# Performance work log

Measured on AMD Instinct MI355X. Metric: run time of the kernel, lower is better.

The kernel has to match this reference:

```python
import jax, jax.numpy as jnp
import numpy as np

H = 16
D_MODEL = 1024
D_K = D_MODEL // H
NWORDS = 16384


def setup_inputs() -> dict:
    key0 = jax.random.key(0)
    ks = jax.random.split(key0, 11)
    s = 0.02
    return {
        "query": jax.random.normal(ks[0], (1, D_MODEL), dtype=jnp.float32),
        "key": jax.random.normal(ks[1], (NWORDS, D_MODEL), dtype=jnp.float32),
        "value": jax.random.normal(ks[2], (NWORDS, D_MODEL), dtype=jnp.float32),
        "Wq": jax.random.normal(ks[3], (D_MODEL, D_MODEL), dtype=jnp.float32) * s,
        "bq": jax.random.normal(ks[4], (D_MODEL,), dtype=jnp.float32) * s,
        "Wk": jax.random.normal(ks[5], (D_MODEL, D_MODEL), dtype=jnp.float32) * s,
        "bk": jax.random.normal(ks[6], (D_MODEL,), dtype=jnp.float32) * s,
        "Wv": jax.random.normal(ks[7], (D_MODEL, D_MODEL), dtype=jnp.float32) * s,
        "bv": jax.random.normal(ks[8], (D_MODEL,), dtype=jnp.float32) * s,
        "Wo": jax.random.normal(ks[9], (D_MODEL, D_MODEL), dtype=jnp.float32) * s,
        "bo": jax.random.normal(ks[10], (D_MODEL,), dtype=jnp.float32) * s,
    }


def reference(query, key, value, Wq, bq, Wk, bk, Wv, bv, Wo, bo):
    # torch Linear: y = x @ W.T + b
    q = (query @ Wq.T + bq).reshape(H, D_K)          # [h, d_k]  (single query token)
    k = (key @ Wk.T + bk).reshape(-1, H, D_K)        # [n, h, d_k]
    v = (value @ Wv.T + bv).reshape(-1, H, D_K)      # [n, h, d_k]
    # NOTE: original module applies NO 1/sqrt(d_k) scaling.
    scores = jnp.einsum("hd,nhd->hn", q, k)          # [h, n]
    p_attn = jax.nn.softmax(scores, axis=-1)          # dropout p=0 -> no-op
    x = jnp.einsum("hn,nhd->hd", p_attn, v).reshape(1, H * D_K)  # [1, d_model]
    return x @ Wo.T + bo                              # [1, d_model]
```

## Files before the change

kernel.cpp:

```cpp
#include <hip/hip_runtime.h>

#define DM 1024
#define NW 16384

typedef __attribute__((ext_vector_type(8))) short short8;
typedef __attribute__((ext_vector_type(4))) float f32x4;

#define OFF_AH   1024
#define OFF_AL   9216
#define OFF_D0   17408
#define OFF_SP   17440
#define OFF_X    25632
#define OFF_W    26656
#define OFF_PART 49152

__device__ __forceinline__ unsigned short f2bf(float f) {
  unsigned int u = __float_as_uint(f);
  return (unsigned short)((u + 0x7fffu + ((u >> 16) & 1u)) >> 16);
}

__global__ __launch_bounds__(256) void k_rowdot(const float* __restrict__ W,
                                                const float* __restrict__ v,
                                                const float* __restrict__ b,
                                                float* __restrict__ out) {
  const int wave = (blockIdx.x * 256 + threadIdx.x) >> 6;
  const int lane = threadIdx.x & 63;
  const float* row = W + (size_t)wave * DM + 4 * lane;
  float s = 0.f;
#pragma unroll
  for (int j = 0; j < 4; ++j) {
    float4 a = *(const float4*)(row + j * 256);
    float4 x = *(const float4*)(v + j * 256 + 4 * lane);
    s += a.x * x.x + a.y * x.y + a.z * x.z + a.w * x.w;
  }
#pragma unroll
  for (int off = 32; off; off >>= 1) s += __shfl_xor(s, off, 64);
  if (lane == 0) out[wave] = s + b[wave];
}

__global__ __launch_bounds__(256) void k_qck(const float* __restrict__ Wq,
                                             const float* __restrict__ bq,
                                             const float* __restrict__ query,
                                             const float* __restrict__ Wk,
                                             const float* __restrict__ bk,
                                             short* __restrict__ Ah,
                                             short* __restrict__ Al,
                                             float* __restrict__ d0,
                                             float* __restrict__ w) {
  const int h = blockIdx.x >> 2;
  const int mc = blockIdx.x & 3;
  const int t = threadIdx.x;
  const int lane = t & 63;
  const int wv = t >> 6;
  __shared__ float qh[64];
  w[blockIdx.x * 256 + t] = 0.f;
  float4 qv[4];
#pragma unroll
  for (int j = 0; j < 4; ++j) qv[j] = *(const float4*)(query + j * 256 + 4 * lane);
#pragma unroll 1
  for (int ii = 0; ii < 16; ii += 4) {
    float4 a[4][4];
#pragma unroll
    for (int r = 0; r < 4; ++r) {
      const float* rp = Wq + (size_t)(h * 64 + 4 * (ii + r) + wv) * DM + 4 * lane;
#pragma unroll
      for (int j = 0; j < 4; ++j) a[r][j] = *(const float4*)(rp + j * 256);
    }
    float s[4] = {0.f, 0.f, 0.f, 0.f};
#pragma unroll
    for (int r = 0; r < 4; ++r)
#pragma unroll
      for (int j = 0; j < 4; ++j)
        s[r] += a[r][j].x * qv[j].x + a[r][j].y * qv[j].y +
                a[r][j].z * qv[j].z + a[r][j].w * qv[j].w;
#pragma unroll
    for (int off = 32; off; off >>= 1)
#pragma unroll
      for (int r = 0; r < 4; ++r) s[r] += __shfl_xor(s[r], off, 64);
    if (lane == 0)
#pragma unroll
      for (int r = 0; r < 4; ++r)
        qh[4 * (ii + r) + wv] = s[r] + bq[h * 64 + 4 * (ii + r) + wv];
  }
  __syncthreads();
  const int m = mc * 256 + t;
  const float* Wp = Wk + (size_t)(h * 64) * DM + m;
  float s = 0.f;
#pragma unroll 2
  for (int db = 0; db < 8; ++db) {
    float wv8[8];
#pragma unroll
    for (int j = 0; j < 8; ++j) wv8[j] = Wp[(size_t)(db * 8 + j) * DM];
#pragma unroll
    for (int j = 0; j < 8; ++j) s = fmaf(qh[db * 8 + j], wv8[j], s);
  }
  unsigned short hu = f2bf(s);
  float hf = __uint_as_float(((unsigned int)hu) << 16);
  unsigned short lu = f2bf(s - hf);
  const int kb = m >> 5, q = (m >> 3) & 3, j = m & 7;
  const int idx = (kb * 64 + q * 16 + h) * 8 + j;
  Ah[idx] = (short)hu;
  Al[idx] = (short)lu;
  if (mc == 0 && t == 0) {
    float tt = 0.f;
    for (int d = 0; d < 64; ++d) tt += qh[d] * bk[h * 64 + d];
    d0[h] = tt;
  }
}

__global__ __launch_bounds__(512, 4) void k_spv(const float* __restrict__ key,
                                                const float* __restrict__ value,
                                                const short* __restrict__ AhG,
                                                const short* __restrict__ AlG,
                                                const float* __restrict__ d0,
                                                float* __restrict__ part,
                                                float* __restrict__ Spart) {
  const int nb = blockIdx.x;
  const int t = threadIdx.x;
  const int lane = t & 63;
  const int wv = t >> 6;
  const int tile = wv >> 2;
  const int kq = wv & 3;
  const int row16 = lane & 15;
  const int nl = tile * 16 + row16;
  const int n = nb * 32 + nl;
  const int quad = lane >> 4;
  const float* base = key + (size_t)n * DM + quad * 8;
  const short8* A8h = (const short8*)AhG;
  const short8* A8l = (const short8*)AlG;
  __shared__ float el[32 * 16];
  __shared__ f32x4 sred[8][64];

  short8 ah[2][4], al[2][4];
  float4 f0[2][4], f1[2][4];
  f32x4 acc0 = {0.f, 0.f, 0.f, 0.f};
  f32x4 acc1 = {0.f, 0.f, 0.f, 0.f};

#define LOADG(buf, g) { \
  _Pragma("unroll") for (int i = 0; i < 4; ++i) { \
    const int kb = kq * 8 + (g) * 4 + i; \
    ah[buf][i] = A8h[kb * 64 + lane]; \
    al[buf][i] = A8l[kb * 64 + lane]; \
    f0[buf][i] = *(const float4*)(base + kb * 32); \
    f1[buf][i] = *(const float4*)(base + kb * 32 + 4); \
  } }

#define PROC(buf) { \
  _Pragma("unroll") for (int i = 0; i < 4; ++i) { \
    float ff[8] = {f0[buf][i].x, f0[buf][i].y, f0[buf][i].z, f0[buf][i].w, \
                   f1[buf][i].x, f1[buf][i].y, f1[buf][i].z, f1[buf][i].w}; \
    short8 bh, bl; \
    _Pragma("unroll") for (int j = 0; j < 8; ++j) { \
      unsigned short hu = f2bf(ff[j]); \
      bh[j] = (short)hu; \
      float hf = __uint_as_float(((unsigned int)hu) << 16); \
      bl[j] = (short)f2bf(ff[j] - hf); \
    } \
    if ((i & 1) == 0) { \
      acc0 = __builtin_amdgcn_mfma_f32_16x16x32_bf16(ah[buf][i], bh, acc0, 0, 0, 0); \
      acc0 = __builtin_amdgcn_mfma_f32_16x16x32_bf16(ah[buf][i], bl, acc0, 0, 0, 0); \
      acc0 = __builtin_amdgcn_mfma_f32_16x16x32_bf16(al[buf][i], bh, acc0, 0, 0, 0); \
    } else { \
      acc1 = __builtin_amdgcn_mfma_f32_16x16x32_bf16(ah[buf][i], bh, acc1, 0, 0, 0); \
      acc1 = __builtin_amdgcn_mfma_f32_16x16x32_bf16(ah[buf][i], bl, acc1, 0, 0, 0); \
      acc1 = __builtin_amdgcn_mfma_f32_16x16x32_bf16(al[buf][i], bh, acc1, 0, 0, 0); \
    } \
  } }

  LOADG(0, 0)
  LOADG(1, 1)
  PROC(0)
  PROC(1)
#undef LOADG
#undef PROC

  f32x4 at = acc0 + acc1;
  sred[wv][lane] = at;
  __syncthreads();
  if (kq == 0) {
    f32x4 o1 = sred[wv + 1][lane];
    f32x4 o2 = sred[wv + 2][lane];
    f32x4 o3 = sred[wv + 3][lane];
    const float4 dv = *(const float4*)(d0 + quad * 4);
    float ex0 = __expf(at[0] + o1[0] + o2[0] + o3[0] + dv.x);
    float ex1 = __expf(at[1] + o1[1] + o2[1] + o3[1] + dv.y);
    float ex2 = __expf(at[2] + o1[2] + o2[2] + o3[2] + dv.z);
    float ex3 = __expf(at[3] + o1[3] + o2[3] + o3[3] + dv.w);
    *(float4*)&el[nl * 16 + quad * 4] = make_float4(ex0, ex1, ex2, ex3);
  }
  __syncthreads();

  if (t < 16) {
    float s = 0.f;
#pragma unroll
    for (int r = 0; r < 32; ++r) s += el[r * 16 + t];
    Spart[t * 512 + nb] = s;
  }

  float2 acc[16];
#pragma unroll
  for (int h = 0; h < 16; ++h) acc[h] = make_float2(0.f, 0.f);
  const float* vp = value + (size_t)(nb * 32) * DM + 2 * t;
  float2 vbA[8], vbB[8];

#define LOADV(VB, G) { _Pragma("unroll") for (int i = 0; i < 8; ++i) \
    VB[i] = *(const float2*)(vp + (size_t)((G) * 8 + i) * DM); }
#define COMPV(VB, G) { \
  _Pragma("unroll") for (int i = 0; i < 8; ++i) { \
    const float4* er4 = (const float4*)&el[((G) * 8 + i) * 16]; \
    float4 e0 = er4[0], e1 = er4[1], e2 = er4[2], e3 = er4[3]; \
    float2 vvv = VB[i]; \
    acc[0].x  = fmaf(e0.x, vvv.x, acc[0].x);  acc[0].y  = fmaf(e0.x, vvv.y, acc[0].y); \
    acc[1].x  = fmaf(e0.y, vvv.x, acc[1].x);  acc[1].y  = fmaf(e0.y, vvv.y, acc[1].y); \
    acc[2].x  = fmaf(e0.z, vvv.x, acc[2].x);  acc[2].y  = fmaf(e0.z, vvv.y, acc[2].y); \
    acc[3].x  = fmaf(e0.w, vvv.x, acc[3].x);  acc[3].y  = fmaf(e0.w, vvv.y, acc[3].y); \
    acc[4].x  = fmaf(e1.x, vvv.x, acc[4].x);  acc[4].y  = fmaf(e1.x, vvv.y, acc[4].y); \
    acc[5].x  = fmaf(e1.y, vvv.x, acc[5].x);  acc[5].y  = fmaf(e1.y, vvv.y, acc[5].y); \
    acc[6].x  = fmaf(e1.z, vvv.x, acc[6].x);  acc[6].y  = fmaf(e1.z, vvv.y, acc[6].y); \
    acc[7].x  = fmaf(e1.w, vvv.x, acc[7].x);  acc[7].y  = fmaf(e1.w, vvv.y, acc[7].y); \
    acc[8].x  = fmaf(e2.x, vvv.x, acc[8].x);  acc[8].y  = fmaf(e2.x, vvv.y, acc[8].y); \
    acc[9].x  = fmaf(e2.y, vvv.x, acc[9].x);  acc[9].y  = fmaf(e2.y, vvv.y, acc[9].y); \
    acc[10].x = fmaf(e2.z, vvv.x, acc[10].x); acc[10].y = fmaf(e2.z, vvv.y, acc[10].y); \
    acc[11].x = fmaf(e2.w, vvv.x, acc[11].x); acc[11].y = fmaf(e2.w, vvv.y, acc[11].y); \
    acc[12].x = fmaf(e3.x, vvv.x, acc[12].x); acc[12].y = fmaf(e3.x, vvv.y, acc[12].y); \
    acc[13].x = fmaf(e3.y, vvv.x, acc[13].x); acc[13].y = fmaf(e3.y, vvv.y, acc[13].y); \
    acc[14].x = fmaf(e3.z, vvv.x, acc[14].x); acc[14].y = fmaf(e3.z, vvv.y, acc[14].y); \
    acc[15].x = fmaf(e3.w, vvv.x, acc[15].x); acc[15].y = fmaf(e3.w, vvv.y, acc[15].y); \
  } }

  LOADV(vbA, 0)
  LOADV(vbB, 1)
  COMPV(vbA, 0) LOADV(vbA, 2)
  COMPV(vbB, 1) LOADV(vbB, 3)
  COMPV(vbA, 2)
  COMPV(vbB, 3)
#undef LOADV
#undef COMPV

  float* pp = part + (size_t)nb * (16 * DM) + 2 * t;
#pragma unroll
  for (int h = 0; h < 16; ++h) *(float2*)(pp + (size_t)h * DM) = acc[h];
}

__global__ __launch_bounds__(256) void k_wred(const float* __restrict__ part,
                                              float* __restrict__ w) {
  const int g = blockIdx.x * 256 + threadIdx.x;
  const int o = g & 16383;
  const int q = g >> 14;
  float s = 0.f;
#pragma unroll 1
  for (int ib = 0; ib < 16; ++ib) {
    float x[8];
#pragma unroll
    for (int j = 0; j < 8; ++j)
      x[j] = part[(size_t)(q * 128 + ib * 8 + j) * 16384 + o];
#pragma unroll
    for (int j = 0; j < 8; ++j) s += x[j];
  }
  atomicAdd(w + o, s);
}

__global__ __launch_bounds__(256) void k_xproj(const float* __restrict__ Wv,
                                               const float* __restrict__ w,
                                               const float* __restrict__ bv,
                                               const float* __restrict__ Spart,
                                               float* __restrict__ x) {
  const int wave = (blockIdx.x * 256 + threadIdx.x) >> 6;
  const int lane = threadIdx.x & 63;
  const int h = wave >> 6;
  const float* vec = w + (size_t)h * DM;
  const float* row = Wv + (size_t)wave * DM + 4 * lane;
  const float* sp = Spart + (size_t)h * 512;
  float s = 0.f, ss = 0.f;
#pragma unroll
  for (int i = 0; i < 8; ++i) ss += sp[i * 64 + lane];
#pragma unroll
  for (int j = 0; j < 4; ++j) {
    float4 a = *(const float4*)(row + j * 256);
    float4 x4 = *(const float4*)(vec + j * 256 + 4 * lane);
    s += a.x * x4.x + a.y * x4.y + a.z * x4.z + a.w * x4.w;
  }
#pragma unroll
  for (int off = 32; off; off >>= 1) {
    s += __shfl_xor(s, off, 64);
    ss += __shfl_xor(ss, off, 64);
  }
  if (lane == 0) x[wave] = s / ss + bv[wave];
}

extern "C" void kernel_launch(void* const* d_in, const int* in_sizes, int n_in,
                              void* d_out, int out_size, void* d_ws, size_t ws_size,
                              hipStream_t stream) {
  const float* query = (const float*)d_in[0];
  const float* key   = (const float*)d_in[1];
  const float* value = (const float*)d_in[2];
  const float* Wq    = (const float*)d_in[3];
  const float* bq    = (const float*)d_in[4];
  const float* Wk    = (const float*)d_in[5];
  const float* bk    = (const float*)d_in[6];
  const float* Wv    = (const float*)d_in[7];
  const float* bv    = (const float*)d_in[8];
  const float* Wo    = (const float*)d_in[9];
  const float* bo    = (const float*)d_in[10];
  float* out = (float*)d_out;
  float* ws  = (float*)d_ws;
  short* Ah  = (short*)(ws + OFF_AH);
  short* Al  = (short*)(ws + OFF_AL);

  k_qck    <<<64,  256, 0, stream>>>(Wq, bq, query, Wk, bk, Ah, Al,
                                     ws + OFF_D0, ws + OFF_W);
  k_spv    <<<512, 512, 0, stream>>>(key, value, Ah, Al, ws + OFF_D0,
                                     ws + OFF_PART, ws + OFF_SP);
  k_wred   <<<256, 256, 0, stream>>>(ws + OFF_PART, ws + OFF_W);
  k_xproj  <<<256, 256, 0, stream>>>(Wv, ws + OFF_W, bv, ws + OFF_SP, ws + OFF_X);
  k_rowdot <<<256, 256, 0, stream>>>(Wo, ws + OFF_X, bo, out);
}
```

Measured before the change: 209.6 us.

## Stream key tiles into LDS via async global_load_lds with multi-stage pipeline

The key-score phase of k_spv now copies key rows straight into a 4-slot shared-memory ring with global_load_lds, using an XOR-swizzled layout, instead of loading them into registers. The K dimension is split into 8 stages of 128 columns, with three loads kept in flight through explicit vmcnt waits, barriers and scheduling barriers. The aim is to cut register pressure and hide global-memory latency behind the split-bf16 MFMA work. In exchange the kernel uses 64 KB of extra LDS, which may lower occupancy, and adds a barrier per stage.

```diff
diff --git a/kernel.cpp b/kernel.cpp
--- a/kernel.cpp
+++ b/kernel.cpp
@@ -18,6 +18,10 @@
   unsigned int u = __float_as_uint(f);
   return (unsigned short)((u + 0x7fffu + ((u >> 16) & 1u)) >> 16);
 }
+
+#define WAITV(N) asm volatile("s_waitcnt vmcnt(" #N ")" ::: "memory")
+#define SB() __builtin_amdgcn_sched_barrier(0)
+#define BAR() { __builtin_amdgcn_s_barrier(); __builtin_amdgcn_sched_barrier(0); }
 
 __global__ __launch_bounds__(256) void k_rowdot(const float* __restrict__ W,
                                                 const float* __restrict__ v,
@@ -123,69 +127,82 @@
   const int kq = wv & 3;
   const int row16 = lane & 15;
   const int nl = tile * 16 + row16;
-  const int n = nb * 32 + nl;
   const int quad = lane >> 4;
-  const float* base = key + (size_t)n * DM + quad * 8;
   const short8* A8h = (const short8*)AhG;
   const short8* A8l = (const short8*)AlG;
+
+  __shared__ float kst[4][32 * 128];
   __shared__ float el[32 * 16];
   __shared__ f32x4 sred[8][64];
 
-  short8 ah[2][4], al[2][4];
-  float4 f0[2][4], f1[2][4];
+  const int slot0 = wv * 2;
+  const int swz = nl & 7;
+  const int c0 = kq * 8 + quad * 2;
+  const int o0 = nl * 128 + ((c0 ^ swz) << 2);
+  const int o1 = nl * 128 + (((c0 + 1) ^ swz) << 2);
+
   f32x4 acc0 = {0.f, 0.f, 0.f, 0.f};
   f32x4 acc1 = {0.f, 0.f, 0.f, 0.f};
-
-#define LOADG(buf, g) { \
-  _Pragma("unroll") for (int i = 0; i < 4; ++i) { \
-    const int kb = kq * 8 + (g) * 4 + i; \
-    ah[buf][i] = A8h[kb * 64 + lane]; \
-    al[buf][i] = A8l[kb * 64 + lane]; \
-    f0[buf][i] = *(const float4*)(base + kb * 32); \
-    f1[buf][i] = *(const float4*)(base + kb * 32 + 4); \
+  short8 a0h, a0l, a1h, a1l, a2h, a2l;
+
+#define STAGE(S) { \
+  _Pragma("unroll") for (int j = 0; j < 2; ++j) { \
+    const int slot = slot0 + j; \
+    const int row = 2 * slot + (lane >> 5); \
+    const int ch = (lane & 31) ^ (row & 7); \
+    const float* g = key + (size_t)(nb * 32 + row) * DM + (S) * 128 + ch * 4; \
+    __builtin_amdgcn_global_load_lds( \
+        (const __attribute__((address_space(1))) void*)g, \
+        (__attribute__((address_space(3))) void*)&kst[(S) & 3][slot * 256], \
+        16, 0, 0); \
   } }
 
-#define PROC(buf) { \
-  _Pragma("unroll") for (int i = 0; i < 4; ++i) { \
-    float ff[8] = {f0[buf][i].x, f0[buf][i].y, f0[buf][i].z, f0[buf][i].w, \
-                   f1[buf][i].x, f1[buf][i].y, f1[buf][i].z, f1[buf][i].w}; \
-    short8 bh, bl; \
-    _Pragma("unroll") for (int j = 0; j < 8; ++j) { \
-      unsigned short hu = f2bf(ff[j]); \
-      bh[j] = (short)hu; \
-      float hf = __uint_as_float(((unsigned int)hu) << 16); \
-      bl[j] = (short)f2bf(ff[j] - hf); \
-    } \
-    if ((i & 1) == 0) { \
-      acc0 = __builtin_amdgcn_mfma_f32_16x16x32_bf16(ah[buf][i], bh, acc0, 0, 0, 0); \
-      acc0 = __builtin_amdgcn_mfma_f32_16x16x32_bf16(ah[buf][i], bl, acc0, 0, 0, 0); \
-      acc0 = __builtin_amdgcn_mfma_f32_16x16x32_bf16(al[buf][i], bh, acc0, 0, 0, 0); \
-    } else { \
-      acc1 = __builtin_amdgcn_mfma_f32_16x16x32_bf16(ah[buf][i], bh, acc1, 0, 0, 0); \
-      acc1 = __builtin_amdgcn_mfma_f32_16x16x32_bf16(ah[buf][i], bl, acc1, 0, 0, 0); \
-      acc1 = __builtin_amdgcn_mfma_f32_16x16x32_bf16(al[buf][i], bh, acc1, 0, 0, 0); \
-    } \
-  } }
-
-  LOADG(0, 0)
-  LOADG(1, 1)
-  PROC(0)
-  PROC(1)
-#undef LOADG
-#undef PROC
+#define A_LD(H, L, S) { H = A8h[((S) * 4 + kq) * 64 + lane]; \
+                        L = A8l[((S) * 4 + kq) * 64 + lane]; }
+
+#define COMP(S, H, L, ACC) { \
+  float4 q0 = *(const float4*)&kst[(S) & 3][o0]; \
+  float4 q1 = *(const float4*)&kst[(S) & 3][o1]; \
+  float ff[8] = {q0.x, q0.y, q0.z, q0.w, q1.x, q1.y, q1.z, q1.w}; \
+  short8 bh, bl; \
+  _Pragma("unroll") for (int j = 0; j < 8; ++j) { \
+    unsigned short hu = f2bf(ff[j]); \
+    bh[j] = (short)hu; \
+    float hf = __uint_as_float(((unsigned int)hu) << 16); \
+    bl[j] = (short)f2bf(ff[j] - hf); \
+  } \
+  ACC = __builtin_amdgcn_mfma_f32_16x16x32_bf16(H, bh, ACC, 0, 0, 0); \
+  ACC = __builtin_amdgcn_mfma_f32_16x16x32_bf16(H, bl, ACC, 0, 0, 0); \
+  ACC = __builtin_amdgcn_mfma_f32_16x16x32_bf16(L, bh, ACC, 0, 0, 0); }
+
+  A_LD(a0h, a0l, 0) STAGE(0) SB();
+  A_LD(a1h, a1l, 1) STAGE(1) SB();
+  A_LD(a2h, a2l, 2) STAGE(2) SB();
+
+  WAITV(8); BAR(); COMP(0, a0h, a0l, acc0) A_LD(a0h, a0l, 3) STAGE(3) SB();
+  WAITV(8); BAR(); COMP(1, a1h, a1l, acc1) A_LD(a1h, a1l, 4) STAGE(4) SB();
+  WAITV(8); BAR(); COMP(2, a2h, a2l, acc0) A_LD(a2h, a2l, 5) STAGE(5) SB();
+  WAITV(8); BAR(); COMP(3, a0h, a0l, acc1) A_LD(a0h, a0l, 6) STAGE(6) SB();
+  WAITV(8); BAR(); COMP(4, a1h, a1l, acc0) A_LD(a1h, a1l, 7) STAGE(7) SB();
+  WAITV(8); BAR(); COMP(5, a2h, a2l, acc1)
+  WAITV(4); BAR(); COMP(6, a0h, a0l, acc0)
+  WAITV(0); BAR(); COMP(7, a1h, a1l, acc1)
+#undef STAGE
+#undef A_LD
+#undef COMP
 
   f32x4 at = acc0 + acc1;
   sred[wv][lane] = at;
   __syncthreads();
   if (kq == 0) {
-    f32x4 o1 = sred[wv + 1][lane];
-    f32x4 o2 = sred[wv + 2][lane];
-    f32x4 o3 = sred[wv + 3][lane];
+    f32x4 o1v = sred[wv + 1][lane];
+    f32x4 o2v = sred[wv + 2][lane];
+    f32x4 o3v = sred[wv + 3][lane];
     const float4 dv = *(const float4*)(d0 + quad * 4);
-    float ex0 = __expf(at[0] + o1[0] + o2[0] + o3[0] + dv.x);
-    float ex1 = __expf(at[1] + o1[1] + o2[1] + o3[1] + dv.y);
-    float ex2 = __expf(at[2] + o1[2] + o2[2] + o3[2] + dv.z);
-    float ex3 = __expf(at[3] + o1[3] + o2[3] + o3[3] + dv.w);
+    float ex0 = __expf(at[0] + o1v[0] + o2v[0] + o3v[0] + dv.x);
+    float ex1 = __expf(at[1] + o1v[1] + o2v[1] + o3v[1] + dv.y);
+    float ex2 = __expf(at[2] + o1v[2] + o2v[2] + o3v[2] + dv.z);
+    float ex3 = __expf(at[3] + o1v[3] + o2v[3] + o3v[3] + dv.w);
     *(float4*)&el[nl * 16 + quad * 4] = make_float4(ex0, ex1, ex2, ex3);
   }
   __syncthreads();
```

Result: slower. 215.8 us (+3.0%).
